# Kernel tuning notes

Hardware: AMD Instinct MI355X
Metric: run time of the kernel (lower is better)

Reference implementation:

```python
import math
import jax, jax.numpy as jnp
import numpy as np

IN_CH = 512
KEY = 512
VAL = 512
B, T = 8, 2048
SQRT_KEY = math.sqrt(float(KEY))


def setup_inputs() -> dict:
    key = jax.random.key(0)
    ks = jax.random.split(key, 7)
    s_in = 1.0 / math.sqrt(IN_CH)
    return {
        "x": jax.random.normal(ks[0], (B, T, IN_CH), dtype=jnp.float32),
        "Wq": jax.random.uniform(ks[1], (IN_CH, KEY), jnp.float32, -s_in, s_in),
        "bq": jax.random.uniform(ks[2], (KEY,), jnp.float32, -s_in, s_in),
        "Wk": jax.random.uniform(ks[3], (IN_CH, KEY), jnp.float32, -s_in, s_in),
        "bk": jax.random.uniform(ks[4], (KEY,), jnp.float32, -s_in, s_in),
        "Wv": jax.random.uniform(ks[5], (IN_CH, VAL), jnp.float32, -s_in, s_in),
        "bv": jax.random.uniform(ks[6], (VAL,), jnp.float32, -s_in, s_in),
    }


def reference(x, Wq, bq, Wk, bk, Wv, bv):
    # x: [B, T, C]
    q = x @ Wq + bq          # [B, T, K]
    k = x @ Wk + bk          # [B, T, K]
    v = x @ Wv + bv          # [B, T, V]
    logits = jnp.einsum("btk,bsk->bts", q, k)  # [B, T(q), T(kv)]
    mask = jnp.tril(jnp.ones((T, T), dtype=bool))  # causal: key s <= query t
    logits = jnp.where(mask[None, :, :], logits, -jnp.inf)
    # NOTE: original torch code softmaxes over dim=1 (the QUERY axis) — kept faithful.
    probs = jax.nn.softmax(logits / SQRT_KEY, axis=1)
    read = jnp.einsum("bts,bsv->btv", probs, v)  # [B, T, V]
    return jnp.concatenate((x, read), axis=2)    # [B, T, C+V]
```

## Files before the change

kernel.cpp:

```cpp
#include <hip/hip_runtime.h>
#include <hip/hip_bf16.h>
#include <math.h>

#define BATCH 8
#define SEQ   2048
#define CH    512
#define ROWS  (BATCH * SEQ)
#define INVSQ 0.044194173824159216f

#define BM 128
#define BK 32
#define TILE_ELEMS (BM * BK)
#define TP 68

typedef __attribute__((ext_vector_type(8))) __bf16 bf16x8;
typedef __attribute__((ext_vector_type(4))) float f32x4;

__device__ inline unsigned short f2bf(float f) {
    unsigned u = __builtin_bit_cast(unsigned, f);
    u += 0x7fffu + ((u >> 16) & 1u);
    return (unsigned short)(u >> 16);
}
__device__ inline float bf2f(unsigned short s) {
    unsigned u = ((unsigned)s) << 16;
    return __builtin_bit_cast(float, u);
}

__device__ __forceinline__ void stage_tile(
    const unsigned short* __restrict__ gbase, size_t stride,
    unsigned short* lds, int wave, int lane)
{
#pragma unroll
    for (int j = 0; j < 2; ++j) {
        int chunk = wave * 2 + j;
        int row = chunk * 16 + (lane >> 2);
        const unsigned short* g = gbase + (size_t)row * stride + ((lane & 3) << 3);
        __builtin_amdgcn_global_load_lds(
            (const __attribute__((address_space(1))) unsigned int*)g,
            (__attribute__((address_space(3))) unsigned int*)(lds + (chunk << 9)),
            16, 0, 0);
    }
}

__device__ __forceinline__ void load_frags(
    const unsigned short* lds, int w0, int l16, int quad, bf16x8* f)
{
#pragma unroll
    for (int r = 0; r < 4; ++r)
        f[r] = *(const bf16x8*)(lds + (w0 + r * 16 + l16) * BK + quad * 8);
}

__global__ __launch_bounds__(256) void fuse_x_kernel(
    const float* __restrict__ x, unsigned short* __restrict__ xb,
    float* __restrict__ out, float* __restrict__ Z)
{
    if (blockIdx.x < 64) Z[blockIdx.x * 256 + threadIdx.x] = 0.f;
    size_t base = ((size_t)blockIdx.x * 256 + threadIdx.x) * 8;
    size_t row = base >> 9, c = base & 511;
    float4 v0 = *(const float4*)(x + base);
    float4 v1 = *(const float4*)(x + base + 4);
    float* o = out + row * 1024 + c;
    *(float4*)o = v0;
    *(float4*)(o + 4) = v1;
    alignas(16) unsigned short t[8];
    t[0] = f2bf(v0.x); t[1] = f2bf(v0.y); t[2] = f2bf(v0.z); t[3] = f2bf(v0.w);
    t[4] = f2bf(v1.x); t[5] = f2bf(v1.y); t[6] = f2bf(v1.z); t[7] = f2bf(v1.w);
    *(uint4*)(xb + base) = *(const uint4*)t;
}

__global__ __launch_bounds__(256) void transpose_w_kernel(
    const float* __restrict__ Wq, const float* __restrict__ Wk,
    const float* __restrict__ Wv, unsigned short* __restrict__ Wt)
{
    __shared__ unsigned short T[64 * TP];
    const int k0 = blockIdx.x * 64, n0 = blockIdx.y * 64, w = blockIdx.z;
    const float* W = (w == 0) ? Wq : (w == 1) ? Wk : Wv;
    const int tid = threadIdx.x;
#pragma unroll
    for (int i = 0; i < 2; ++i) {
        int slot = tid + i * 256;
        int kr = slot >> 3, c8 = (slot & 7) << 3;
        float4 a = *(const float4*)(W + (size_t)(k0 + kr) * CH + n0 + c8);
        float4 b = *(const float4*)(W + (size_t)(k0 + kr) * CH + n0 + c8 + 4);
        T[(c8 + 0) * TP + kr] = f2bf(a.x); T[(c8 + 1) * TP + kr] = f2bf(a.y);
        T[(c8 + 2) * TP + kr] = f2bf(a.z); T[(c8 + 3) * TP + kr] = f2bf(a.w);
        T[(c8 + 4) * TP + kr] = f2bf(b.x); T[(c8 + 5) * TP + kr] = f2bf(b.y);
        T[(c8 + 6) * TP + kr] = f2bf(b.z); T[(c8 + 7) * TP + kr] = f2bf(b.w);
    }
    __syncthreads();
#pragma unroll
    for (int i = 0; i < 2; ++i) {
        int slot = tid + i * 256;
        int nr = slot >> 3, k8 = (slot & 7) << 3;
        uint2 lo = *(const uint2*)(T + nr * TP + k8);
        uint2 hi = *(const uint2*)(T + nr * TP + k8 + 4);
        uint4 u; u.x = lo.x; u.y = lo.y; u.z = hi.x; u.w = hi.y;
        *(uint4*)(Wt + ((size_t)w * CH + n0 + nr) * CH + k0 + k8) = u;
    }
}

__global__ __launch_bounds__(256) void transpose_v_kernel(
    const unsigned short* __restrict__ vb, const float* __restrict__ Z,
    unsigned short* __restrict__ Vt)
{
    __shared__ unsigned short T[64 * TP];
    const int s0 = blockIdx.x * 64, v0 = blockIdx.y * 64, b = blockIdx.z;
    const int tid = threadIdx.x;
#pragma unroll
    for (int i = 0; i < 2; ++i) {
        int slot = tid + i * 256;
        int sr = slot >> 3, c8 = (slot & 7) << 3;
        float inv = 1.0f / Z[b * SEQ + s0 + sr];
        uint4 raw = *(const uint4*)(vb + ((size_t)b * SEQ + s0 + sr) * CH + v0 + c8);
        const unsigned short* p = (const unsigned short*)&raw;
#pragma unroll
        for (int j = 0; j < 8; ++j)
            T[(c8 + j) * TP + sr] = f2bf(bf2f(p[j]) * inv);
    }
    __syncthreads();
#pragma unroll
    for (int i = 0; i < 2; ++i) {
        int slot = tid + i * 256;
        int vr = slot >> 3, s8 = (slot & 7) << 3;
        uint2 lo = *(const uint2*)(T + vr * TP + s8);
        uint2 hi = *(const uint2*)(T + vr * TP + s8 + 4);
        uint4 u; u.x = lo.x; u.y = lo.y; u.z = hi.x; u.w = hi.y;
        *(uint4*)(Vt + ((size_t)b * CH + v0 + vr) * SEQ + s0 + s8) = u;
    }
}

__global__ __launch_bounds__(256) void qkv_kernel(
    const unsigned short* __restrict__ xb, const unsigned short* __restrict__ Wt,
    const float* __restrict__ bq, const float* __restrict__ bk,
    const float* __restrict__ bv, unsigned short* __restrict__ qkv)
{
    __shared__ unsigned short As[2 * TILE_ELEMS];
    __shared__ unsigned short Bs[2 * TILE_ELEMS];
    const int xrow0 = blockIdx.x * BM;
    const int wrow0 = blockIdx.y * BM;
    const int tid = threadIdx.x;
    const int lane = tid & 63, wave = tid >> 6;
    const int wm = (wave >> 1) * 64, wn = (wave & 1) * 64;
    const int quad = lane >> 4, l16 = lane & 15;

    f32x4 acc[4][4] = {};
    for (int kk = 0; kk < CH; kk += 64) {
        stage_tile(Wt + (size_t)wrow0 * CH + kk,      CH, As,              wave, lane);
        stage_tile(Wt + (size_t)wrow0 * CH + kk + 32, CH, As + TILE_ELEMS, wave, lane);
        stage_tile(xb + (size_t)xrow0 * CH + kk,      CH, Bs,              wave, lane);
        stage_tile(xb + (size_t)xrow0 * CH + kk + 32, CH, Bs + TILE_ELEMS, wave, lane);
        __syncthreads();
#pragma unroll
        for (int h = 0; h < 2; ++h) {
            bf16x8 a[4], bb[4];
            load_frags(As + h * TILE_ELEMS, wm, l16, quad, a);
            load_frags(Bs + h * TILE_ELEMS, wn, l16, quad, bb);
#pragma unroll
            for (int r = 0; r < 4; ++r)
#pragma unroll
                for (int c = 0; c < 4; ++c)
                    acc[r][c] = __builtin_amdgcn_mfma_f32_16x16x32_bf16(a[r], bb[c], acc[r][c], 0, 0, 0);
        }
        __syncthreads();
    }
    const int which = wrow0 >> 9;
    const float* bias = (which == 0) ? bq : (which == 1) ? bk : bv;
    const float scale = (which == 0) ? INVSQ : 1.0f;
    unsigned short* outw = qkv + (size_t)which * ROWS * CH;
    const int colblk = wrow0 & 511;
#pragma unroll
    for (int r = 0; r < 4; ++r) {
        int colb = colblk + wm + r * 16 + quad * 4;
        float4 b4 = *(const float4*)(bias + colb);
#pragma unroll
        for (int c = 0; c < 4; ++c) {
            int m = xrow0 + wn + c * 16 + l16;
            alignas(8) unsigned short pk[4];
            pk[0] = f2bf((acc[r][c][0] + b4.x) * scale);
            pk[1] = f2bf((acc[r][c][1] + b4.y) * scale);
            pk[2] = f2bf((acc[r][c][2] + b4.z) * scale);
            pk[3] = f2bf((acc[r][c][3] + b4.w) * scale);
            *(uint2*)(outw + (size_t)m * CH + colb) = *(const uint2*)pk;
        }
    }
}

__global__ __launch_bounds__(256) void logits_kernel(
    const unsigned short* __restrict__ qb, const unsigned short* __restrict__ kb,
    unsigned short* __restrict__ E, float* __restrict__ Z)
{
    __shared__ unsigned short As[2 * TILE_ELEMS];
    __shared__ unsigned short Bs[2 * TILE_ELEMS];
    const int id = blockIdx.x;
    const int b = id & 7;
    const int i = id >> 3;
    int tt = (int)((sqrtf(8.f * (float)i + 1.f) - 1.f) * 0.5f);
    int st = i - ((tt * (tt + 1)) >> 1);
    while (st < 0)  { --tt; st = i - ((tt * (tt + 1)) >> 1); }
    while (st > tt) { ++tt; st = i - ((tt * (tt + 1)) >> 1); }
    const int m0s = st * BM;
    const int n0t = tt * BM;
    const int tid = threadIdx.x;
    const int lane = tid & 63, wave = tid >> 6;
    const int wm = (wave >> 1) * 64, wn = (wave & 1) * 64;
    const int quad = lane >> 4, l16 = lane & 15;
    const unsigned short* kB = kb + (size_t)b * SEQ * CH;
    const unsigned short* qB = qb + (size_t)b * SEQ * CH;

    f32x4 acc[4][4] = {};
    for (int kk = 0; kk < CH; kk += 64) {
        stage_tile(kB + (size_t)m0s * CH + kk,      CH, As,              wave, lane);
        stage_tile(kB + (size_t)m0s * CH + kk + 32, CH, As + TILE_ELEMS, wave, lane);
        stage_tile(qB + (size_t)n0t * CH + kk,      CH, Bs,              wave, lane);
        stage_tile(qB + (size_t)n0t * CH + kk + 32, CH, Bs + TILE_ELEMS, wave, lane);
        __syncthreads();
#pragma unroll
        for (int h = 0; h < 2; ++h) {
            bf16x8 a[4], bb[4];
            load_frags(As + h * TILE_ELEMS, wm, l16, quad, a);
            load_frags(Bs + h * TILE_ELEMS, wn, l16, quad, bb);
#pragma unroll
            for (int r = 0; r < 4; ++r)
#pragma unroll
                for (int c = 0; c < 4; ++c)
                    acc[r][c] = __builtin_amdgcn_mfma_f32_16x16x32_bf16(a[r], bb[c], acc[r][c], 0, 0, 0);
        }
        __syncthreads();
    }
#pragma unroll
    for (int r = 0; r < 4; ++r) {
        int sb = m0s + wm + r * 16 + quad * 4;
        float ev[4][4];
#pragma unroll
        for (int c = 0; c < 4; ++c) {
            int t = n0t + wn + c * 16 + l16;
#pragma unroll
            for (int reg = 0; reg < 4; ++reg)
                ev[c][reg] = (sb + reg <= t) ? __expf(acc[r][c][reg]) : 0.f;
        }
#pragma unroll
        for (int reg = 0; reg < 4; ++reg) {
            float z = ev[0][reg] + ev[1][reg] + ev[2][reg] + ev[3][reg];
            z += __shfl_xor(z, 1);
            z += __shfl_xor(z, 2);
            z += __shfl_xor(z, 4);
            z += __shfl_xor(z, 8);
            if (l16 == 0) atomicAdd(&Z[b * SEQ + sb + reg], z);
        }
#pragma unroll
        for (int c = 0; c < 4; ++c) {
            int t = n0t + wn + c * 16 + l16;
            alignas(8) unsigned short pk[4];
            pk[0] = f2bf(ev[c][0]); pk[1] = f2bf(ev[c][1]);
            pk[2] = f2bf(ev[c][2]); pk[3] = f2bf(ev[c][3]);
            *(uint2*)(E + ((size_t)b * SEQ + t) * SEQ + sb) = *(const uint2*)pk;
        }
    }
}

__global__ __launch_bounds__(256) void read_kernel(
    const unsigned short* __restrict__ E, const unsigned short* __restrict__ Vt,
    float* __restrict__ out)
{
    __shared__ unsigned short As[2 * TILE_ELEMS];
    __shared__ unsigned short Bs[2 * TILE_ELEMS];
    const int id = blockIdx.x;
    const int b = id & 7;
    const int rem = id >> 3;
    const int mv = rem & 3;
    const int r0 = rem >> 2;
    const int tt = (r0 < 8) ? r0 : 23 - r0;
    const int m0v = mv * BM;
    const int n0t = tt * BM;
    const int Kmax = (tt + 1) * BM;
    const int tid = threadIdx.x;
    const int lane = tid & 63, wave = tid >> 6;
    const int wm = (wave >> 1) * 64, wn = (wave & 1) * 64;
    const int quad = lane >> 4, l16 = lane & 15;
    const unsigned short* Vb = Vt + (size_t)b * CH * SEQ;
    const unsigned short* Eb = E + (size_t)b * SEQ * SEQ;

    f32x4 acc[4][4] = {};
    for (int kk = 0; kk < Kmax; kk += 64) {
        stage_tile(Vb + (size_t)m0v * SEQ + kk,      SEQ, As,              wave, lane);
        stage_tile(Vb + (size_t)m0v * SEQ + kk + 32, SEQ, As + TILE_ELEMS, wave, lane);
        stage_tile(Eb + (size_t)n0t * SEQ + kk,      SEQ, Bs,              wave, lane);
        stage_tile(Eb + (size_t)n0t * SEQ + kk + 32, SEQ, Bs + TILE_ELEMS, wave, lane);
        __syncthreads();
#pragma unroll
        for (int h = 0; h < 2; ++h) {
            bf16x8 a[4], bb[4];
            load_frags(As + h * TILE_ELEMS, wm, l16, quad, a);
            load_frags(Bs + h * TILE_ELEMS, wn, l16, quad, bb);
#pragma unroll
            for (int r = 0; r < 4; ++r)
#pragma unroll
                for (int c = 0; c < 4; ++c)
                    acc[r][c] = __builtin_amdgcn_mfma_f32_16x16x32_bf16(a[r], bb[c], acc[r][c], 0, 0, 0);
        }
        __syncthreads();
    }
#pragma unroll
    for (int r = 0; r < 4; ++r) {
        int v = 512 + m0v + wm + r * 16 + quad * 4;
#pragma unroll
        for (int c = 0; c < 4; ++c) {
            int t = n0t + wn + c * 16 + l16;
            float4 f;
            f.x = acc[r][c][0]; f.y = acc[r][c][1];
            f.z = acc[r][c][2]; f.w = acc[r][c][3];
            *(float4*)(out + ((size_t)b * SEQ + t) * 1024 + v) = f;
        }
    }
}

extern "C" void kernel_launch(void* const* d_in, const int* in_sizes, int n_in,
                              void* d_out, int out_size, void* d_ws, size_t ws_size,
                              hipStream_t stream) {
    const float* x  = (const float*)d_in[0];
    const float* Wq = (const float*)d_in[1];
    const float* bq = (const float*)d_in[2];
    const float* Wk = (const float*)d_in[3];
    const float* bk = (const float*)d_in[4];
    const float* Wv = (const float*)d_in[5];
    const float* bv = (const float*)d_in[6];
    float* out = (float*)d_out;

    char* ws = (char*)d_ws;
    const size_t QKV_BYTES = (size_t)ROWS * CH * 2;
    const size_t E_BYTES   = (size_t)BATCH * SEQ * SEQ * 2;
    unsigned short* qkv = (unsigned short*)ws;
    unsigned short* qb = qkv;
    unsigned short* kb = (unsigned short*)(ws + QKV_BYTES);
    unsigned short* vb = (unsigned short*)(ws + 2 * QKV_BYTES);
    unsigned short* E  = (unsigned short*)(ws + 3 * QKV_BYTES);
    float* Z = (float*)(ws + 3 * QKV_BYTES + E_BYTES);
    unsigned short* xb = E;
    unsigned short* Wt = (unsigned short*)((char*)E + QKV_BYTES);
    unsigned short* Vt = qb;

    dim3 blk(256);
    fuse_x_kernel<<<dim3(4096), blk, 0, stream>>>(x, xb, out, Z);
    transpose_w_kernel<<<dim3(8, 8, 3), blk, 0, stream>>>(Wq, Wk, Wv, Wt);
    qkv_kernel<<<dim3(128, 12), blk, 0, stream>>>(xb, Wt, bq, bk, bv, qkv);
    logits_kernel<<<dim3(1088), blk, 0, stream>>>(qb, kb, E, Z);
    transpose_v_kernel<<<dim3(32, 8, 8), blk, 0, stream>>>(vb, Z, Vt);
    read_kernel<<<dim3(512), blk, 0, stream>>>(E, Vt, out);
}
```

Measured before the change: 236.9 us.

## Rewrite QKV GEMM with 8-wave blocks and async global-to-LDS double buffering

Replaces the QKV projection GEMM with a 512-thread kernel that computes 128x256 tiles. It stages tiles straight into LDS via global_load_lds with a swizzled layout and double buffers across the K loop. MFMA bursts are interleaved with prefetches of later K-slices using explicit waitcnt, barriers, setprio and a XCD-aware block remap, so load latency is meant to hide behind compute. The cost is more manual synchronisation, which is fragile, and added register pressure for 2 blocks per CU. The QKV GEMM is only one of several kernels, so any change to total time is limited to its share.

After: 230.0 us. 1.03x faster.

```diff
diff --git a/kernel.cpp b/kernel.cpp
--- a/kernel.cpp
+++ b/kernel.cpp
@@ -129,40 +129,106 @@
     }
 }
 
-__global__ __launch_bounds__(256) void qkv_kernel(
+#define MFMA_ROW(r, af) \
+    acc[r][0] = __builtin_amdgcn_mfma_f32_16x16x32_bf16(af, b0, acc[r][0], 0, 0, 0); \
+    acc[r][1] = __builtin_amdgcn_mfma_f32_16x16x32_bf16(af, b1, acc[r][1], 0, 0, 0); \
+    acc[r][2] = __builtin_amdgcn_mfma_f32_16x16x32_bf16(af, b2, acc[r][2], 0, 0, 0); \
+    acc[r][3] = __builtin_amdgcn_mfma_f32_16x16x32_bf16(af, b3, acc[r][3], 0, 0, 0);
+
+__global__ __launch_bounds__(512, 2) void qkv8_kernel(
     const unsigned short* __restrict__ xb, const unsigned short* __restrict__ Wt,
     const float* __restrict__ bq, const float* __restrict__ bk,
     const float* __restrict__ bv, unsigned short* __restrict__ qkv)
 {
-    __shared__ unsigned short As[2 * TILE_ELEMS];
-    __shared__ unsigned short Bs[2 * TILE_ELEMS];
-    const int xrow0 = blockIdx.x * BM;
-    const int wrow0 = blockIdx.y * BM;
+    __shared__ unsigned short lds[24576];
     const int tid = threadIdx.x;
     const int lane = tid & 63, wave = tid >> 6;
-    const int wm = (wave >> 1) * 64, wn = (wave & 1) * 64;
+    const int waveA = wave >> 2;
+    const int waveB = wave & 3;
     const int quad = lane >> 4, l16 = lane & 15;
 
+    int id = (int)blockIdx.x;
+    id = (id & 7) * 96 + (id >> 3);
+    const int xt = id / 12, wt = id - xt * 12;
+    const int xrow0 = xt << 8, wrow0 = wt << 7;
+
+    const unsigned short* __restrict__ Wg = Wt + (size_t)wrow0 * CH;
+    const unsigned short* __restrict__ Xg = xb + (size_t)xrow0 * CH;
+
+    const int srow = tid >> 2;
+    const int scol = (((tid & 3) ^ ((tid >> 3) & 3)) << 3);
+    const size_t ga  = (size_t)srow * CH + scol;
+    const size_t gb1 = (size_t)(srow + 128) * CH + scol;
+    const int wdst = wave * 512;
+    const int rswz = ((quad ^ ((l16 >> 1) & 3)) << 3);
+    const int arow = waveA * 64 + l16;
+    const int brow = waveB * 64 + l16;
+
     f32x4 acc[4][4] = {};
-    for (int kk = 0; kk < CH; kk += 64) {
-        stage_tile(Wt + (size_t)wrow0 * CH + kk,      CH, As,              wave, lane);
-        stage_tile(Wt + (size_t)wrow0 * CH + kk + 32, CH, As + TILE_ELEMS, wave, lane);
-        stage_tile(xb + (size_t)xrow0 * CH + kk,      CH, Bs,              wave, lane);
-        stage_tile(xb + (size_t)xrow0 * CH + kk + 32, CH, Bs + TILE_ELEMS, wave, lane);
-        __syncthreads();
-#pragma unroll
-        for (int h = 0; h < 2; ++h) {
-            bf16x8 a[4], bb[4];
-            load_frags(As + h * TILE_ELEMS, wm, l16, quad, a);
-            load_frags(Bs + h * TILE_ELEMS, wn, l16, quad, bb);
-#pragma unroll
-            for (int r = 0; r < 4; ++r)
-#pragma unroll
-                for (int c = 0; c < 4; ++c)
-                    acc[r][c] = __builtin_amdgcn_mfma_f32_16x16x32_bf16(a[r], bb[c], acc[r][c], 0, 0, 0);
-        }
-        __syncthreads();
-    }
+
+    auto stageA = [&](int V) {
+        if (V >= 16) return;
+        const unsigned short* g = Wg + ga + V * 32;
+        unsigned short* d = lds + (V & 1) * 4096 + wdst;
+        __builtin_amdgcn_global_load_lds(
+            (const __attribute__((address_space(1))) unsigned int*)g,
+            (__attribute__((address_space(3))) unsigned int*)d, 16, 0, 0);
+    };
+    auto stageB = [&](int V) {
+        if (V >= 16) return;
+        const unsigned short* g0 = Xg + ga + V * 32;
+        const unsigned short* g1 = Xg + gb1 + V * 32;
+        unsigned short* d = lds + 8192 + (V & 1) * 8192 + wdst;
+        __builtin_amdgcn_global_load_lds(
+            (const __attribute__((address_space(1))) unsigned int*)g0,
+            (__attribute__((address_space(3))) unsigned int*)d, 16, 0, 0);
+        __builtin_amdgcn_global_load_lds(
+            (const __attribute__((address_space(1))) unsigned int*)g1,
+            (__attribute__((address_space(3))) unsigned int*)(d + 4096), 16, 0, 0);
+    };
+
+    stageA(0); stageB(0); stageB(1);
+    asm volatile("s_waitcnt vmcnt(2)" ::: "memory");
+    __builtin_amdgcn_s_barrier();
+    __builtin_amdgcn_sched_barrier(0);
+
+#pragma unroll
+    for (int U = 0; U < 16; ++U) {
+        const unsigned short* Ab = lds + (U & 1) * 4096;
+        const unsigned short* Bb = lds + 8192 + (U & 1) * 8192;
+        bf16x8 a0, a1, b0, b1, b2, b3;
+        b0 = *(const bf16x8*)(Bb + (brow +  0) * 32 + rswz);
+        b1 = *(const bf16x8*)(Bb + (brow + 16) * 32 + rswz);
+        b2 = *(const bf16x8*)(Bb + (brow + 32) * 32 + rswz);
+        b3 = *(const bf16x8*)(Bb + (brow + 48) * 32 + rswz);
+        a0 = *(const bf16x8*)(Ab + (arow +  0) * 32 + rswz);
+        a1 = *(const bf16x8*)(Ab + (arow + 16) * 32 + rswz);
+        stageA(U + 1);
+        __builtin_amdgcn_s_barrier();
+        asm volatile("s_waitcnt lgkmcnt(0)" ::: "memory");
+        __builtin_amdgcn_sched_barrier(0);
+        __builtin_amdgcn_s_setprio(1);
+        MFMA_ROW(0, a0);
+        MFMA_ROW(1, a1);
+        __builtin_amdgcn_s_setprio(0);
+        __builtin_amdgcn_s_barrier();
+        __builtin_amdgcn_sched_barrier(0);
+        a0 = *(const bf16x8*)(Ab + (arow + 32) * 32 + rswz);
+        a1 = *(const bf16x8*)(Ab + (arow + 48) * 32 + rswz);
+        stageB(U + 2);
+        __builtin_amdgcn_s_barrier();
+        asm volatile("s_waitcnt lgkmcnt(0)" ::: "memory");
+        __builtin_amdgcn_sched_barrier(0);
+        __builtin_amdgcn_s_setprio(1);
+        MFMA_ROW(2, a0);
+        MFMA_ROW(3, a1);
+        __builtin_amdgcn_s_setprio(0);
+        if (U <= 13)      asm volatile("s_waitcnt vmcnt(2)" ::: "memory");
+        else if (U == 14) asm volatile("s_waitcnt vmcnt(0)" ::: "memory");
+        __builtin_amdgcn_s_barrier();
+        __builtin_amdgcn_sched_barrier(0);
+    }
+
     const int which = wrow0 >> 9;
     const float* bias = (which == 0) ? bq : (which == 1) ? bk : bv;
     const float scale = (which == 0) ? INVSQ : 1.0f;
@@ -170,11 +236,11 @@
     const int colblk = wrow0 & 511;
 #pragma unroll
     for (int r = 0; r < 4; ++r) {
-        int colb = colblk + wm + r * 16 + quad * 4;
+        int colb = colblk + waveA * 64 + r * 16 + quad * 4;
         float4 b4 = *(const float4*)(bias + colb);
 #pragma unroll
         for (int c = 0; c < 4; ++c) {
-            int m = xrow0 + wn + c * 16 + l16;
+            int m = xrow0 + waveB * 64 + c * 16 + l16;
             alignas(8) unsigned short pk[4];
             pk[0] = f2bf((acc[r][c][0] + b4.x) * scale);
             pk[1] = f2bf((acc[r][c][1] + b4.y) * scale);
@@ -184,6 +250,7 @@
         }
     }
 }
+#undef MFMA_ROW
 
 __global__ __launch_bounds__(256) void logits_kernel(
     const unsigned short* __restrict__ qb, const unsigned short* __restrict__ kb,
@@ -342,7 +409,7 @@
     dim3 blk(256);
     fuse_x_kernel<<<dim3(4096), blk, 0, stream>>>(x, xb, out, Z);
     transpose_w_kernel<<<dim3(8, 8, 3), blk, 0, stream>>>(Wq, Wk, Wv, Wt);
-    qkv_kernel<<<dim3(128, 12), blk, 0, stream>>>(xb, Wt, bq, bk, bv, qkv);
+    qkv8_kernel<<<dim3(768), dim3(512), 0, stream>>>(xb, Wt, bq, bk, bv, qkv);
     logits_kernel<<<dim3(1088), blk, 0, stream>>>(qb, kb, E, Z);
     transpose_v_kernel<<<dim3(32, 8, 8), blk, 0, stream>>>(vb, Z, Vt);
     read_kernel<<<dim3(512), blk, 0, stream>>>(E, Vt, out);
```
